# Optimization experiments

Measured on AMD Instinct MI355X. Metric: run time of the kernel, lower is better.

The kernel has to match this reference:

```python
import jax, jax.numpy as jnp
import numpy as np

RESOLUTION = 2 ** 8  # 256
N_POINTS = 2 ** 21


def setup_inputs() -> dict:
    key = jax.random.key(0)
    k1, k2 = jax.random.split(key)
    inp = jax.random.uniform(k1, (N_POINTS, 3), dtype=jnp.float32)
    grid = jax.random.normal(k2, (RESOLUTION, RESOLUTION, RESOLUTION, 3), dtype=jnp.float32) * 0.01
    return {"input": inp, "feature_params": grid}


def reference(input, feature_params):
    R = feature_params.shape[0]
    scaled = input * (R - 1)
    lower = jnp.clip(jnp.floor(scaled).astype(jnp.int32), 0, R - 2)
    upper = jnp.clip(lower + 1, 0, R - 1)
    t = scaled - lower.astype(scaled.dtype)
    xl, yl, zl = lower[:, 0], lower[:, 1], lower[:, 2]
    xu, yu, zu = upper[:, 0], upper[:, 1], upper[:, 2]
    tx, ty, tz = t[:, 0:1], t[:, 1:2], t[:, 2:3]  # (N,1) for broadcast over channels
    # note original indexes grid as [z, y, x]
    c000 = feature_params[zl, yl, xl]
    c001 = feature_params[zl, yl, xu]
    c010 = feature_params[zl, yu, xl]
    c011 = feature_params[zl, yu, xu]
    c100 = feature_params[zu, yl, xl]
    c101 = feature_params[zu, yl, xu]
    c110 = feature_params[zu, yu, xl]
    c111 = feature_params[zu, yu, xu]
    c00 = c000 * (1 - tx) + c001 * tx
    c01 = c010 * (1 - tx) + c011 * tx
    c10 = c100 * (1 - tx) + c101 * tx
    c11 = c110 * (1 - tx) + c111 * tx
    c0 = c00 * (1 - ty) + c01 * ty
    c1 = c10 * (1 - ty) + c11 * ty
    return c0 * (1 - tz) + c1 * tz
```

## Files before the change

### kernel.cpp

```cpp
#include <hip/hip_runtime.h>


#define NB     8192
#define CAP    512u
#define GBLK   512
#define CHUNKF 100
#define NCHUNK 81
#define NF4    2025
#define LDSF   8100

#define CUR_OFF   67108864u
#define NEEDED    (67108864u + 32768u)

typedef float f4v __attribute__((ext_vector_type(4)));
typedef float f2v __attribute__((ext_vector_type(2)));
typedef f4v f4u __attribute__((aligned(8)));
typedef f2v f2u __attribute__((aligned(8)));

__device__ __forceinline__ void cell_of(float p, int& l, float& t) {
    float s = p * 255.0f;
    int v = (int)floorf(s);
    v = v < 0 ? 0 : (v > 254 ? 254 : v);
    l = v;
    t = s - (float)v;
}

__device__ __forceinline__ int fine_bin3(float px, float py, float pz) {
    int xl, yl, zl; float tx, ty, tz;
    cell_of(px, xl, tx);
    cell_of(py, yl, ty);
    cell_of(pz, zl, tz);
    return ((zl >> 3) << 8) | ((yl >> 3) << 3) | (xl >> 5);
}

__device__ __forceinline__ void direct_lerp(const float* __restrict__ grid,
                                            float* __restrict__ out, int i,
                                            int xl, int yl, int zl,
                                            float tx, float ty, float tz) {
    int b00 = (zl * 65536 + yl * 256 + xl) * 3;
    int b01 = b00 + 768, b10 = b00 + 196608, b11 = b10 + 768;
    float s00[6], s01[6], s10[6], s11[6];
#pragma unroll
    for (int k = 0; k < 6; ++k) s00[k] = grid[b00 + k];
#pragma unroll
    for (int k = 0; k < 6; ++k) s01[k] = grid[b01 + k];
#pragma unroll
    for (int k = 0; k < 6; ++k) s10[k] = grid[b10 + k];
#pragma unroll
    for (int k = 0; k < 6; ++k) s11[k] = grid[b11 + k];
#pragma unroll
    for (int c = 0; c < 3; ++c) {
        float c00 = s00[c] * (1.0f - tx) + s00[c + 3] * tx;
        float c01 = s01[c] * (1.0f - tx) + s01[c + 3] * tx;
        float c10 = s10[c] * (1.0f - tx) + s10[c + 3] * tx;
        float c11 = s11[c] * (1.0f - tx) + s11[c + 3] * tx;
        float c0 = c00 * (1.0f - ty) + c01 * ty;
        float c1 = c10 * (1.0f - ty) + c11 * ty;
        out[3 * i + c] = c0 * (1.0f - tz) + c1 * tz;
    }
}

__global__ __launch_bounds__(1024) void k_init(unsigned* __restrict__ cur) {
    int i = blockIdx.x * 1024 + threadIdx.x;
    if (i < NB) cur[i] = (unsigned)i * CAP;
}

__global__ __launch_bounds__(1024) void k_scatter(const float* __restrict__ inp,
                                                  const float* __restrict__ grid,
                                                  float4* __restrict__ binned,
                                                  unsigned* __restrict__ cur,
                                                  float* __restrict__ out, int n) {
    __shared__ unsigned cnt[NB];
    __shared__ unsigned base[NB];
    int t = threadIdx.x;
    int P = n >> 1;
    int stride = gridDim.x * 1024;
    int iters = (P + stride - 1) / stride;

    if ((n & 1) && blockIdx.x == 0 && t == 0) {
        int i = n - 1;
        float px = inp[3 * i], py = inp[3 * i + 1], pz = inp[3 * i + 2];
        int b = fine_bin3(px, py, pz);
        unsigned r = atomicAdd(&cur[b], 1u);
        if (r - (unsigned)b * CAP < CAP) {
            float4 v; v.x = px; v.y = py; v.z = pz; v.w = __uint_as_float((unsigned)i);
            binned[r] = v;
        } else {
            int xl, yl, zl; float tx, ty, tz;
            cell_of(px, xl, tx); cell_of(py, yl, ty); cell_of(pz, zl, tz);
            direct_lerp(grid, out, i, xl, yl, zl, tx, ty, tz);
        }
    }

    for (int it = 0; it < iters; ++it) {
        int pr = it * stride + blockIdx.x * 1024 + t;
        for (int k = t; k < NB; k += 1024) cnt[k] = 0;
        __syncthreads();
        int b0 = 0, b1 = 0; unsigned r0 = 0, r1 = 0;
        float4 p0, p1;
        bool valid = (pr < P);
        if (valid) {
            f4v a = *(const f4u*)(inp + 6 * pr);
            f2v b = *(const f2u*)(inp + 6 * pr + 4);
            p0.x = a.x; p0.y = a.y; p0.z = a.z;
            p0.w = __uint_as_float((unsigned)(2 * pr));
            p1.x = a.w; p1.y = b.x; p1.z = b.y;
            p1.w = __uint_as_float((unsigned)(2 * pr + 1));
            b0 = fine_bin3(p0.x, p0.y, p0.z);
            b1 = fine_bin3(p1.x, p1.y, p1.z);
            r0 = atomicAdd(&cnt[b0], 1u);
            r1 = atomicAdd(&cnt[b1], 1u);
        }
        __syncthreads();
        for (int k = t; k < NB; k += 1024)
            if (cnt[k]) base[k] = atomicAdd(&cur[k], cnt[k]);
        __syncthreads();
        if (valid) {
            unsigned s0 = base[b0] + r0;
            unsigned s1 = base[b1] + r1;
            if (s0 - (unsigned)b0 * CAP < CAP) binned[s0] = p0;
            else {
                int xl, yl, zl; float tx, ty, tz;
                cell_of(p0.x, xl, tx); cell_of(p0.y, yl, ty); cell_of(p0.z, zl, tz);
                direct_lerp(grid, out, 2 * pr, xl, yl, zl, tx, ty, tz);
            }
            if (s1 - (unsigned)b1 * CAP < CAP) binned[s1] = p1;
            else {
                int xl, yl, zl; float tx, ty, tz;
                cell_of(p1.x, xl, tx); cell_of(p1.y, yl, ty); cell_of(p1.z, zl, tz);
                direct_lerp(grid, out, 2 * pr + 1, xl, yl, zl, tx, ty, tz);
            }
        }
        __syncthreads();
    }
}

__global__ __launch_bounds__(GBLK, 8) void k_gather(const float4* __restrict__ binned,
                                                    const float* __restrict__ grid,
                                                    const unsigned* __restrict__ cur,
                                                    float* __restrict__ out) {
    __shared__ __align__(16) float slab[LDSF];
    int bin = ((blockIdx.x & 7) << 10) | (blockIdx.x >> 3);
    int x0 = (bin & 7) << 5;
    int y0 = ((bin >> 3) & 31) << 3;
    int z0 = (bin >> 8) << 3;
    int t = threadIdx.x;

    unsigned start = (unsigned)bin * CAP;
    unsigned count = cur[bin] - start;
    if (count > CAP) count = CAP;

    float4 v;
    if ((unsigned)t < count) v = binned[start + (unsigned)t];

    for (int u = t; u < NF4; u += GBLK) {
        int chunk = u / 25;
        int j = u - chunk * 25;
        int zc = chunk / 9;
        int yc = chunk - zc * 9;
        int zg = z0 + zc; zg = zg > 255 ? 255 : zg;
        int yg = y0 + yc; yg = yg > 255 ? 255 : yg;
        int joff = (j == 24 && x0 == 224) ? 0 : (j << 2);
        const float* src = grid + (size_t)((zg << 16) | (yg << 8) | x0) * 3 + joff;
        __builtin_amdgcn_global_load_lds(
            (const __attribute__((address_space(1))) unsigned int*)src,
            (__attribute__((address_space(3))) unsigned int*)&slab[(size_t)u * 4],
            16, 0, 0);
    }
    __syncthreads();

    unsigned p = (unsigned)t;
    while (p < count) {
        float px = v.x, py = v.y, pz = v.z;
        unsigned idx = __float_as_uint(v.w);
        p += (unsigned)GBLK;
        if (p < count) v = binned[start + p];

        int xl, yl, zl; float tx, ty, tz;
        cell_of(px, xl, tx);
        cell_of(py, yl, ty);
        cell_of(pz, zl, tz);
        int xc = xl - x0, yc = yl - y0, zc = zl - z0;

        int r0 = (zc * 9 + yc) * CHUNKF + xc * 3;
        int e = r0 & ~1;
        bool d = (r0 & 1) != 0;

#define SEG_READ(b, s)                                   \
        do {                                             \
            f2v q0 = *(const f2u*)(&slab[(b)]);          \
            f2v q1 = *(const f2u*)(&slab[(b) + 2]);      \
            f2v q2 = *(const f2u*)(&slab[(b) + 4]);      \
            f2v q3 = *(const f2u*)(&slab[(b) + 6]);      \
            s[0] = d ? q0.y : q0.x;                      \
            s[1] = d ? q1.x : q0.y;                      \
            s[2] = d ? q1.y : q1.x;                      \
            s[3] = d ? q2.x : q1.y;                      \
            s[4] = d ? q2.y : q2.x;                      \
            s[5] = d ? q3.x : q2.y;                      \
        } while (0)

        float s00[6], s01[6], s10[6], s11[6];
        SEG_READ(e,               s00);
        SEG_READ(e + CHUNKF,      s01);
        SEG_READ(e + 9 * CHUNKF,  s10);
        SEG_READ(e + 10 * CHUNKF, s11);
#undef SEG_READ

        float o[3];
#pragma unroll
        for (int c = 0; c < 3; ++c) {
            float c00 = s00[c] * (1.0f - tx) + s00[c + 3] * tx;
            float c01 = s01[c] * (1.0f - tx) + s01[c + 3] * tx;
            float c10 = s10[c] * (1.0f - tx) + s10[c + 3] * tx;
            float c11 = s11[c] * (1.0f - tx) + s11[c + 3] * tx;
            float c0 = c00 * (1.0f - ty) + c01 * ty;
            float c1 = c10 * (1.0f - ty) + c11 * ty;
            o[c] = c0 * (1.0f - tz) + c1 * tz;
        }
        float3 w; w.x = o[0]; w.y = o[1]; w.z = o[2];
        *(float3*)(out + 3 * (size_t)idx) = w;
    }
}

__global__ __launch_bounds__(256) void k_direct(const float* __restrict__ inp,
                                                const float* __restrict__ grid,
                                                float* __restrict__ out, int n) {
    int i = blockIdx.x * blockDim.x + threadIdx.x;
    if (i >= n) return;
    int xl, yl, zl; float tx, ty, tz;
    cell_of(inp[3 * i + 0], xl, tx);
    cell_of(inp[3 * i + 1], yl, ty);
    cell_of(inp[3 * i + 2], zl, tz);
    direct_lerp(grid, out, i, xl, yl, zl, tx, ty, tz);
}

extern "C" void kernel_launch(void* const* d_in, const int* in_sizes, int n_in,
                              void* d_out, int out_size, void* d_ws, size_t ws_size,
                              hipStream_t stream) {
    const float* inp  = (const float*)d_in[0];
    const float* grid = (const float*)d_in[1];
    float* out = (float*)d_out;
    int n = in_sizes[0] / 3;

    if (ws_size < (size_t)NEEDED) {
        int blocks = (n + 255) / 256;
        k_direct<<<blocks, 256, 0, stream>>>(inp, grid, out, n);
        return;
    }

    char* ws = (char*)d_ws;
    float4*   binned = (float4*)ws;
    unsigned* cur    = (unsigned*)(ws + CUR_OFF);

    k_init   <<<8,   1024, 0, stream>>>(cur);
    k_scatter<<<256, 1024, 0, stream>>>(inp, grid, binned, cur, out, n);
    k_gather <<<NB,  GBLK, 0, stream>>>(binned, grid, cur, out);
}
```

Measured before the change: 141.4 us.

## Make gather persistent over 16 bins with double-buffered LDS slab prefetch

Each gather block now processes 16 consecutive bins instead of one. While the current bin is interpolated, the grid slab for the next bin is staged into a second LDS buffer with global_load_lds, hiding slab load latency and cutting block launch count. The scatter launch grid is also doubled to 512 blocks. Costs are doubled LDS per block (about 64KB), which lowers occupancy, plus the loss of the per-point binned prefetch, and only 512 gather blocks remain for the whole GPU.

```diff
diff --git a/kernel.cpp b/kernel.cpp
--- a/kernel.cpp
+++ b/kernel.cpp
@@ -4,6 +4,7 @@
 #define NB     8192
 #define CAP    512u
 #define GBLK   512
+#define BPB    16
 #define CHUNKF 100
 #define NCHUNK 81
 #define NF4    2025
@@ -135,91 +136,101 @@
     }
 }
 
-__global__ __launch_bounds__(GBLK, 8) void k_gather(const float4* __restrict__ binned,
-                                                    const float* __restrict__ grid,
-                                                    const unsigned* __restrict__ cur,
-                                                    float* __restrict__ out) {
-    __shared__ __align__(16) float slab[LDSF];
-    int bin = ((blockIdx.x & 7) << 10) | (blockIdx.x >> 3);
-    int x0 = (bin & 7) << 5;
-    int y0 = ((bin >> 3) & 31) << 3;
-    int z0 = (bin >> 8) << 3;
+#define STAGE_SLAB(binv, dst)                                                   \
+    do {                                                                        \
+        int x0_ = ((binv) & 7) << 5;                                            \
+        int y0_ = (((binv) >> 3) & 31) << 3;                                    \
+        int z0_ = ((binv) >> 8) << 3;                                           \
+        for (int u = t; u < NF4; u += GBLK) {                                   \
+            int chunk = u / 25;                                                 \
+            int j = u - chunk * 25;                                             \
+            int zc = chunk / 9;                                                 \
+            int yc = chunk - zc * 9;                                            \
+            int zg = z0_ + zc; zg = zg > 255 ? 255 : zg;                        \
+            int yg = y0_ + yc; yg = yg > 255 ? 255 : yg;                        \
+            int joff = (j == 24 && x0_ == 224) ? 0 : (j << 2);                  \
+            const float* src =                                                  \
+                grid + (size_t)((zg << 16) | (yg << 8) | x0_) * 3 + joff;       \
+            __builtin_amdgcn_global_load_lds(                                   \
+                (const __attribute__((address_space(1))) unsigned int*)src,     \
+                (__attribute__((address_space(3))) unsigned int*)&(dst)[(size_t)u * 4], \
+                16, 0, 0);                                                      \
+        }                                                                       \
+    } while (0)
+
+__global__ __launch_bounds__(GBLK) void k_gather(const float4* __restrict__ binned,
+                                                 const float* __restrict__ grid,
+                                                 const unsigned* __restrict__ cur,
+                                                 float* __restrict__ out) {
+    __shared__ __align__(16) float slab[2][LDSF];
     int t = threadIdx.x;
-
-    unsigned start = (unsigned)bin * CAP;
-    unsigned count = cur[bin] - start;
-    if (count > CAP) count = CAP;
-
-    float4 v;
-    if ((unsigned)t < count) v = binned[start + (unsigned)t];
-
-    for (int u = t; u < NF4; u += GBLK) {
-        int chunk = u / 25;
-        int j = u - chunk * 25;
-        int zc = chunk / 9;
-        int yc = chunk - zc * 9;
-        int zg = z0 + zc; zg = zg > 255 ? 255 : zg;
-        int yg = y0 + yc; yg = yg > 255 ? 255 : yg;
-        int joff = (j == 24 && x0 == 224) ? 0 : (j << 2);
-        const float* src = grid + (size_t)((zg << 16) | (yg << 8) | x0) * 3 + joff;
-        __builtin_amdgcn_global_load_lds(
-            (const __attribute__((address_space(1))) unsigned int*)src,
-            (__attribute__((address_space(3))) unsigned int*)&slab[(size_t)u * 4],
-            16, 0, 0);
-    }
-    __syncthreads();
-
-    unsigned p = (unsigned)t;
-    while (p < count) {
-        float px = v.x, py = v.y, pz = v.z;
-        unsigned idx = __float_as_uint(v.w);
-        p += (unsigned)GBLK;
-        if (p < count) v = binned[start + p];
-
-        int xl, yl, zl; float tx, ty, tz;
-        cell_of(px, xl, tx);
-        cell_of(py, yl, ty);
-        cell_of(pz, zl, tz);
-        int xc = xl - x0, yc = yl - y0, zc = zl - z0;
-
-        int r0 = (zc * 9 + yc) * CHUNKF + xc * 3;
-        int e = r0 & ~1;
-        bool d = (r0 & 1) != 0;
-
-#define SEG_READ(b, s)                                   \
-        do {                                             \
-            f2v q0 = *(const f2u*)(&slab[(b)]);          \
-            f2v q1 = *(const f2u*)(&slab[(b) + 2]);      \
-            f2v q2 = *(const f2u*)(&slab[(b) + 4]);      \
-            f2v q3 = *(const f2u*)(&slab[(b) + 6]);      \
-            s[0] = d ? q0.y : q0.x;                      \
-            s[1] = d ? q1.x : q0.y;                      \
-            s[2] = d ? q1.y : q1.x;                      \
-            s[3] = d ? q2.x : q1.y;                      \
-            s[4] = d ? q2.y : q2.x;                      \
-            s[5] = d ? q3.x : q2.y;                      \
-        } while (0)
-
-        float s00[6], s01[6], s10[6], s11[6];
-        SEG_READ(e,               s00);
-        SEG_READ(e + CHUNKF,      s01);
-        SEG_READ(e + 9 * CHUNKF,  s10);
-        SEG_READ(e + 10 * CHUNKF, s11);
+    int sb = ((blockIdx.x & 7) << 6) | (blockIdx.x >> 3);
+    int bin0 = sb * BPB;
+
+    STAGE_SLAB(bin0, slab[0]);
+
+    for (int k = 0; k < BPB; ++k) {
+        int bin = bin0 + k;
+        int cb = k & 1;
+        __syncthreads();
+        if (k + 1 < BPB) STAGE_SLAB(bin + 1, slab[cb ^ 1]);
+
+        int x0 = (bin & 7) << 5;
+        int y0 = ((bin >> 3) & 31) << 3;
+        int z0 = (bin >> 8) << 3;
+        unsigned start = (unsigned)bin * CAP;
+        unsigned count = cur[bin] - start;
+        if (count > CAP) count = CAP;
+
+        for (unsigned p = (unsigned)t; p < count; p += (unsigned)GBLK) {
+            float4 v = binned[start + p];
+            unsigned idx = __float_as_uint(v.w);
+
+            int xl, yl, zl; float tx, ty, tz;
+            cell_of(v.x, xl, tx);
+            cell_of(v.y, yl, ty);
+            cell_of(v.z, zl, tz);
+            int xc = xl - x0, yc = yl - y0, zc = zl - z0;
+
+            int r0 = (zc * 9 + yc) * CHUNKF + xc * 3;
+            int e = r0 & ~1;
+            bool d = (r0 & 1) != 0;
+
+#define SEG_READ(b, s)                                       \
+            do {                                             \
+                f2v q0 = *(const f2u*)(&slab[cb][(b)]);      \
+                f2v q1 = *(const f2u*)(&slab[cb][(b) + 2]);  \
+                f2v q2 = *(const f2u*)(&slab[cb][(b) + 4]);  \
+                f2v q3 = *(const f2u*)(&slab[cb][(b) + 6]);  \
+                s[0] = d ? q0.y : q0.x;                      \
+                s[1] = d ? q1.x : q0.y;                      \
+                s[2] = d ? q1.y : q1.x;                      \
+                s[3] = d ? q2.x : q1.y;                      \
+                s[4] = d ? q2.y : q2.x;                      \
+                s[5] = d ? q3.x : q2.y;                      \
+            } while (0)
+
+            float s00[6], s01[6], s10[6], s11[6];
+            SEG_READ(e,               s00);
+            SEG_READ(e + CHUNKF,      s01);
+            SEG_READ(e + 9 * CHUNKF,  s10);
+            SEG_READ(e + 10 * CHUNKF, s11);
 #undef SEG_READ
 
-        float o[3];
-#pragma unroll
-        for (int c = 0; c < 3; ++c) {
-            float c00 = s00[c] * (1.0f - tx) + s00[c + 3] * tx;
-            float c01 = s01[c] * (1.0f - tx) + s01[c + 3] * tx;
-            float c10 = s10[c] * (1.0f - tx) + s10[c + 3] * tx;
-            float c11 = s11[c] * (1.0f - tx) + s11[c + 3] * tx;
-            float c0 = c00 * (1.0f - ty) + c01 * ty;
-            float c1 = c10 * (1.0f - ty) + c11 * ty;
-            o[c] = c0 * (1.0f - tz) + c1 * tz;
-        }
-        float3 w; w.x = o[0]; w.y = o[1]; w.z = o[2];
-        *(float3*)(out + 3 * (size_t)idx) = w;
+            float o[3];
+#pragma unroll
+            for (int c = 0; c < 3; ++c) {
+                float c00 = s00[c] * (1.0f - tx) + s00[c + 3] * tx;
+                float c01 = s01[c] * (1.0f - tx) + s01[c + 3] * tx;
+                float c10 = s10[c] * (1.0f - tx) + s10[c + 3] * tx;
+                float c11 = s11[c] * (1.0f - tx) + s11[c + 3] * tx;
+                float c0 = c00 * (1.0f - ty) + c01 * ty;
+                float c1 = c10 * (1.0f - ty) + c11 * ty;
+                o[c] = c0 * (1.0f - tz) + c1 * tz;
+            }
+            float3 w; w.x = o[0]; w.y = o[1]; w.z = o[2];
+            *(float3*)(out + 3 * (size_t)idx) = w;
+        }
     }
 }
 
@@ -253,7 +264,7 @@
     float4*   binned = (float4*)ws;
     unsigned* cur    = (unsigned*)(ws + CUR_OFF);
 
-    k_init   <<<8,   1024, 0, stream>>>(cur);
-    k_scatter<<<256, 1024, 0, stream>>>(inp, grid, binned, cur, out, n);
-    k_gather <<<NB,  GBLK, 0, stream>>>(binned, grid, cur, out);
-}
+    k_init   <<<8,        1024, 0, stream>>>(cur);
+    k_scatter<<<512,      1024, 0, stream>>>(inp, grid, binned, cur, out, n);
+    k_gather <<<NB / BPB, GBLK, 0, stream>>>(binned, grid, cur, out);
+}
```

Measured after the change: 143.9 us. No clear change (+1.8%).
